# Performance work log

Measured on AMD Instinct MI355X. Metric: run time of the kernel, lower is better.

Reference implementation:

```python
import jax, jax.numpy as jnp
import numpy as np

KH, KW = 3, 3
PAD = 1
STRIDE = 1


def dht1(x):
    # 1D Discrete Hartley Transform along last axis: Re(FFT) - Im(FFT)
    f = jnp.fft.fft(x, axis=-1)
    return f.real - f.imag


def dht2(x, fft_h, fft_w):
    # zero-pad trailing two dims up to (fft_h, fft_w), then DHT along w then h
    pad_h = fft_h - x.shape[-2]
    pad_w = fft_w - x.shape[-1]
    pads = [(0, 0)] * (x.ndim - 2) + [(0, pad_h), (0, pad_w)]
    x = jnp.pad(x, pads)
    x = dht1(x)
    x = jnp.swapaxes(dht1(jnp.swapaxes(x, -1, -2)), -1, -2)
    return x


def setup_inputs() -> dict:
    key = jax.random.key(0)
    k1, k2 = jax.random.split(key)
    x = jax.random.normal(k1, (8, 64, 128, 128), dtype=jnp.float32)
    weight = jax.random.normal(k2, (64, 64, KH, KW), dtype=jnp.float32)
    return {"x": x, "weight": weight}


def reference(x, weight):
    b, c_in, h, w = x.shape
    out_h = (h + 2 * PAD - KH) // STRIDE + 1
    out_w = (w + 2 * PAD - KW) // STRIDE + 1
    x_p = jnp.pad(x, ((0, 0), (0, 0), (PAD, PAD), (PAD, PAD)))
    fft_h = h + 2 * PAD + KH - 1
    fft_w = w + 2 * PAD + KW - 1

    x_ht = dht2(x_p, fft_h, fft_w)          # [B, Cin, fh, fw]
    w_ht = dht2(weight, fft_h, fft_w)        # [Cout, Cin, fh, fw]

    x_f = jnp.flip(x_ht, axis=(-2, -1))
    w_f = jnp.flip(w_ht, axis=(-2, -1))

    # Fused combine + sum over Cin: avoids [B,Cout,Cin,fh,fw] intermediates.
    t1 = jnp.einsum('bchw,ochw->bohw', x_ht, w_ht)
    t2 = jnp.einsum('bchw,ochw->bohw', x_ht, w_f)
    t3 = jnp.einsum('bchw,ochw->bohw', x_f, w_ht)
    t4 = jnp.einsum('bchw,ochw->bohw', x_f, w_f)
    out_ht = (t1 + t2 + t3 - t4) * 0.5

    # idht2 in the source applies only the 1/n scaling twice (no transform)
    output = out_ht / jnp.asarray(fft_h * fft_w, dtype=out_ht.dtype)
    return output[:, :, :out_h, :out_w]
```

## Files before the change

### kernel.cpp

```cpp
#include <hip/hip_runtime.h>
#include <hip/hip_fp16.h>


#define SCALE (0.5f / 17424.0f)
#define MFMA  __builtin_amdgcn_mfma_f32_16x16x32_f16

typedef __attribute__((ext_vector_type(8))) _Float16 f16x8;
typedef __attribute__((ext_vector_type(4))) _Float16 f16x4;
typedef __attribute__((ext_vector_type(4))) float    f32x4;

__global__ __launch_bounds__(512, 4) void dht2_prep(
    const float* __restrict__ x, const float* __restrict__ w,
    _Float16* __restrict__ X, _Float16* __restrict__ cfT,
    _Float16* __restrict__ hgT)
{
    const int tid = threadIdx.x;
    const float step = 6.28318530717958647692f / 132.0f;

    if (blockIdx.x >= 512) {
        const int bid2 = blockIdx.x - 512;
        if (bid2 == 66) {
            if (tid < 128) {
                const int v = tid;
                float s, c;
                _Float16 o[8];
                o[0] = (_Float16)1.0f; o[3] = (_Float16)1.0f;
                o[6] = (_Float16)0.0f; o[7] = (_Float16)0.0f;
                sincosf((float)((v * 1) % 132) * step, &s, &c);       o[1] = (_Float16)(c + s);
                sincosf((float)((v * 2) % 132) * step, &s, &c);       o[2] = (_Float16)(c + s);
                sincosf((float)(((v + 1) * 1) % 132) * step, &s, &c); o[4] = (_Float16)(c - s);
                sincosf((float)(((v + 1) * 2) % 132) * step, &s, &c); o[5] = (_Float16)(c - s);
                *(f16x8*)(cfT + v * 8) = *(f16x8*)o;
            }
            return;
        }
        const int u = bid2;
        float a[3], ap[3];
        a[0] = 1.f; ap[0] = 1.f;
        #pragma unroll
        for (int i = 1; i < 3; ++i) {
            float s, c;
            sincosf((float)((u * i) % 132) * step, &s, &c);
            a[i] = c + s;
            sincosf((float)(((u + 1) * i) % 132) * step, &s, &c);
            ap[i] = c - s;
        }
        for (int it = 0; it < 8; ++it) {
            const int oc = it * 512 + tid;
            const float* wp = w + (size_t)oc * 9;
            float w9[9];
            #pragma unroll
            for (int q = 0; q < 9; ++q) w9[q] = wp[q];
            #pragma unroll
            for (int j = 0; j < 3; ++j) {
                const float h = a[0]*w9[j] + a[1]*w9[3+j] + a[2]*w9[6+j];
                const float g = ap[0]*w9[j] + ap[1]*w9[3+j] + ap[2]*w9[6+j];
                hgT[((size_t)u * 6 + j)     * 4096 + oc] = (_Float16)h;
                hgT[((size_t)u * 6 + 3 + j) * 4096 + oc] = (_Float16)g;
            }
        }
        return;
    }

    const int bc = blockIdx.x;
    const int wv = tid >> 6, lane = tid & 63;
    const int col = lane & 15, quad = lane >> 4;
    __shared__ _Float16 Tfl[144][136];
    __shared__ _Float16 Y1l[144][136];
    __shared__ float castab[132];

    const float* xp = x + (size_t)bc * 16384;
    const int ic = wv * 16 + col;

    float4 xv[4][2];
    #pragma unroll
    for (int kc = 0; kc < 4; ++kc) {
        const int k0 = kc * 32 + quad * 8;
        xv[kc][0] = *(const float4*)(xp + ic * 128 + k0);
        xv[kc][1] = *(const float4*)(xp + ic * 128 + k0 + 4);
    }
    if (tid < 132) {
        float s, c;
        sincosf((float)tid * step, &s, &c);
        castab[tid] = c + s;
    }
    __syncthreads();
    #pragma unroll
    for (int s = 0; s < 36; ++s) {
        const int idx = s * 512 + tid;
        const int row = idx >> 7;
        const int ci  = idx & 127;
        float v = 0.f;
        if (row < 132) v = castab[(row * (ci + 1)) % 132];
        Tfl[row][ci] = (_Float16)v;
    }
    f16x8 bfA[4];
    #pragma unroll
    for (int kc = 0; kc < 4; ++kc) {
        f16x8 t;
        t[0] = (_Float16)xv[kc][0].x; t[1] = (_Float16)xv[kc][0].y;
        t[2] = (_Float16)xv[kc][0].z; t[3] = (_Float16)xv[kc][0].w;
        t[4] = (_Float16)xv[kc][1].x; t[5] = (_Float16)xv[kc][1].y;
        t[6] = (_Float16)xv[kc][1].z; t[7] = (_Float16)xv[kc][1].w;
        bfA[kc] = t;
    }
    __syncthreads();

    f32x4 accA[9];
    #pragma unroll
    for (int mt = 0; mt < 9; ++mt) accA[mt] = (f32x4)0.f;
    #pragma unroll
    for (int kc = 0; kc < 4; ++kc) {
        const int k0 = kc * 32 + quad * 8;
        #pragma unroll
        for (int mt = 0; mt < 9; ++mt) {
            const f16x8 af = *(const f16x8*)&Tfl[mt * 16 + col][k0];
            accA[mt] = MFMA(af, bfA[kc], accA[mt], 0, 0, 0);
        }
    }
    #pragma unroll
    for (int mt = 0; mt < 9; ++mt)
        #pragma unroll
        for (int r = 0; r < 4; ++r)
            Y1l[mt * 16 + quad * 4 + r][ic] = (_Float16)accA[mt][r];
    __syncthreads();

    f32x4 accB[9];
    #pragma unroll
    for (int mt = 0; mt < 9; ++mt) accB[mt] = (f32x4)0.f;
    #pragma unroll
    for (int kc = 0; kc < 4; ++kc) {
        const int k0 = kc * 32 + quad * 8;
        const f16x8 bf = *(const f16x8*)&Y1l[wv * 16 + col][k0];
        #pragma unroll
        for (int mt = 0; mt < 9; ++mt) {
            const f16x8 af = *(const f16x8*)&Tfl[mt * 16 + col][k0];
            accB[mt] = MFMA(af, bf, accB[mt], 0, 0, 0);
        }
    }
    f32x4 accT[3];
    #pragma unroll
    for (int j = 0; j < 3; ++j) accT[j] = (f32x4)0.f;
    if (wv < 4) {
        #pragma unroll
        for (int kc = 0; kc < 4; ++kc) {
            const int k0 = kc * 32 + quad * 8;
            const f16x8 bf = *(const f16x8*)&Y1l[128 + col][k0];
            #pragma unroll
            for (int j = 0; j < 3; ++j) {
                if (j < 2 || wv == 0) {
                    const int mt = (j == 2) ? 8 : (wv * 2 + j);
                    const f16x8 af = *(const f16x8*)&Tfl[mt * 16 + col][k0];
                    accT[j] = MFMA(af, bf, accT[j], 0, 0, 0);
                }
            }
        }
    }
    __syncthreads();

    #pragma unroll
    for (int mt = 0; mt < 9; ++mt)
        #pragma unroll
        for (int r = 0; r < 4; ++r)
            Tfl[mt * 16 + quad * 4 + r][wv * 16 + col] = (_Float16)accB[mt][r];
    if (wv < 4 && col < 4) {
        #pragma unroll
        for (int j = 0; j < 3; ++j) {
            if (j < 2 || wv == 0) {
                const int mt = (j == 2) ? 8 : (wv * 2 + j);
                #pragma unroll
                for (int r = 0; r < 4; ++r)
                    Tfl[mt * 16 + quad * 4 + r][128 + col] = (_Float16)accT[j][r];
            }
        }
    }
    __syncthreads();
    _Float16* Xp = X + (size_t)bc * 17952;
    #pragma unroll
    for (int s = 0; s < 5; ++s) {
        const int ch = tid + 512 * s;
        if (ch < 2244) {
            const int u = ch / 17, kk = ch - u * 17;
            *(f16x8*)(Xp + u * 136 + kk * 8) = *(const f16x8*)&Tfl[u][kk * 8];
        }
    }
}

__global__ __launch_bounds__(256, 2) void combine_mfma(
    const _Float16* __restrict__ X, const _Float16* __restrict__ hgT,
    const _Float16* __restrict__ cfT, float* __restrict__ out)
{
    const int uidx = blockIdx.x;
    const int b = blockIdx.y;
    const int tid = threadIdx.x;
    const int wv = tid >> 6, lane = tid & 63;
    const int col = lane & 15, quad = lane >> 4;
    const int u2 = 131 - uidx;
    const bool doB = (uidx >= 4);

    __shared__ _Float16 Ps[132][72];
    __shared__ _Float16 Ms[132][72];

    {
        const int c = tid >> 2, sub = tid & 3;
        const _Float16* rowd = X + (size_t)(b * 64 + c) * 17952 + (size_t)uidx * 136;
        const _Float16* rowm = X + (size_t)(b * 64 + c) * 17952 + (size_t)u2 * 136;
        #pragma unroll
        for (int k = 0; k < 8; ++k) {
            const int v0 = sub * 32 + 4 * k;
            const f16x4 d = *(const f16x4*)(rowd + v0);
            const f16x4 m = *(const f16x4*)(rowm + (128 - v0));
            #pragma unroll
            for (int i = 0; i < 4; ++i) {
                Ps[v0 + i][c] = d[i] + m[3 - i];
                Ms[v0 + i][c] = d[i] - m[3 - i];
            }
        }
        if (sub == 0) {
            const f16x4 d = *(const f16x4*)(rowd + 128);
            const f16x4 m = *(const f16x4*)(rowm);
            #pragma unroll
            for (int i = 0; i < 4; ++i) {
                Ps[128 + i][c] = d[i] + m[3 - i];
                Ms[128 + i][c] = d[i] - m[3 - i];
            }
        }
    }

    const _Float16* hgu = hgT + (size_t)uidx * 6 * 4096;
    const int orow = wv * 16 + col;
    f16x8 hA[3][2], gA[3][2];
    #pragma unroll
    for (int kt = 0; kt < 3; ++kt)
        #pragma unroll
        for (int hf = 0; hf < 2; ++hf) {
            hA[kt][hf] = *(const f16x8*)(hgu + ((size_t)kt * 64 + orow) * 64 + hf * 32 + quad * 8);
            gA[kt][hf] = *(const f16x8*)(hgu + ((size_t)(3 + kt) * 64 + orow) * 64 + hf * 32 + quad * 8);
        }
    __syncthreads();

    float* outA = out + (((size_t)(b * 64 + wv * 16 + quad * 4)) * 128 + uidx) * 128 + col;
    float* outB = out + (((size_t)(b * 64 + wv * 16 + quad * 4)) * 128 + u2) * 128 + col;

    #pragma unroll
    for (int nt = 0; nt < 8; ++nt) {
        const int vA = nt * 16 + col;
        const int vB = 131 - vA;
        const f16x8 cf8 = *(const f16x8*)(cfT + (size_t)(nt * 16 + col) * 8);
        const float c1 = (float)cf8[1], c2 = (float)cf8[2];
        const float d1 = (float)cf8[4], d2 = (float)cf8[5];
        {
            const f16x8 p0 = *(const f16x8*)&Ps[vA][quad * 8];
            const f16x8 p1 = *(const f16x8*)&Ps[vA][32 + quad * 8];
            const f16x8 m0 = *(const f16x8*)&Ms[vA][quad * 8];
            const f16x8 m1 = *(const f16x8*)&Ms[vA][32 + quad * 8];
            f32x4 aP0 = (f32x4)0.f, aP1 = (f32x4)0.f, aP2 = (f32x4)0.f;
            f32x4 aM0 = (f32x4)0.f, aM1 = (f32x4)0.f, aM2 = (f32x4)0.f;
            aP0 = MFMA(hA[0][0], p0, aP0, 0, 0, 0); aP0 = MFMA(hA[0][1], p1, aP0, 0, 0, 0);
            aP1 = MFMA(hA[1][0], p0, aP1, 0, 0, 0); aP1 = MFMA(hA[1][1], p1, aP1, 0, 0, 0);
            aP2 = MFMA(hA[2][0], p0, aP2, 0, 0, 0); aP2 = MFMA(hA[2][1], p1, aP2, 0, 0, 0);
            aM0 = MFMA(gA[0][0], m0, aM0, 0, 0, 0); aM0 = MFMA(gA[0][1], m1, aM0, 0, 0, 0);
            aM1 = MFMA(gA[1][0], m0, aM1, 0, 0, 0); aM1 = MFMA(gA[1][1], m1, aM1, 0, 0, 0);
            aM2 = MFMA(gA[2][0], m0, aM2, 0, 0, 0); aM2 = MFMA(gA[2][1], m1, aM2, 0, 0, 0);
            #pragma unroll
            for (int r = 0; r < 4; ++r)
                outA[(size_t)r * 16384 + nt * 16] =
                    ((aP0[r] + c1 * aP1[r] + c2 * aP2[r]) +
                     (aM0[r] + d1 * aM1[r] + d2 * aM2[r])) * SCALE;
        }
        if (doB) {
            const f16x8 p0 = *(const f16x8*)&Ps[vB][quad * 8];
            const f16x8 p1 = *(const f16x8*)&Ps[vB][32 + quad * 8];
            const f16x8 m0 = *(const f16x8*)&Ms[vB][quad * 8];
            const f16x8 m1 = *(const f16x8*)&Ms[vB][32 + quad * 8];
            f32x4 bP0 = (f32x4)0.f, bP1 = (f32x4)0.f, bP2 = (f32x4)0.f;
            f32x4 bM0 = (f32x4)0.f, bM1 = (f32x4)0.f, bM2 = (f32x4)0.f;
            bP0 = MFMA(gA[0][0], p0, bP0, 0, 0, 0); bP0 = MFMA(gA[0][1], p1, bP0, 0, 0, 0);
            bP1 = MFMA(gA[1][0], p0, bP1, 0, 0, 0); bP1 = MFMA(gA[1][1], p1, bP1, 0, 0, 0);
            bP2 = MFMA(gA[2][0], p0, bP2, 0, 0, 0); bP2 = MFMA(gA[2][1], p1, bP2, 0, 0, 0);
            bM0 = MFMA(hA[0][0], m0, bM0, 0, 0, 0); bM0 = MFMA(hA[0][1], m1, bM0, 0, 0, 0);
            bM1 = MFMA(hA[1][0], m0, bM1, 0, 0, 0); bM1 = MFMA(hA[1][1], m1, bM1, 0, 0, 0);
            bM2 = MFMA(hA[2][0], m0, bM2, 0, 0, 0); bM2 = MFMA(hA[2][1], m1, bM2, 0, 0, 0);
            #pragma unroll
            for (int r = 0; r < 4; ++r)
                outB[(size_t)r * 16384 + nt * 16] =
                    ((bP0[r] + c1 * bP1[r] + c2 * bP2[r]) -
                     (bM0[r] + d1 * bM1[r] + d2 * bM2[r])) * SCALE;
        }
    }
}

extern "C" void kernel_launch(void* const* d_in, const int* in_sizes, int n_in,
                              void* d_out, int out_size, void* d_ws, size_t ws_size,
                              hipStream_t stream)
{
    const float* x = (const float*)d_in[0];
    const float* w = (const float*)d_in[1];
    char* ws = (char*)d_ws;
    _Float16* cfT = (_Float16*)(ws + 36864);
    _Float16* X   = (_Float16*)(ws + 65536);
    _Float16* hgT = (_Float16*)(ws + 18448384);

    dht2_prep<<<dim3(579), dim3(512), 0, stream>>>(x, w, X, cfT, hgT);

    combine_mfma<<<dim3(66, 8), dim3(256), 0, stream>>>(
        X, hgT, cfT, (float*)d_out);
}
```

Baseline: 110.7 us.

## Spread weight transform across image blocks and strength-reduce DHT table fill

Folds the separate weight-transform and twiddle-table blocks into the 512 image-transform blocks, so each block does one or two slices of the weight work instead of a few tail blocks doing eight slices each. Replaces the per-element modulo in the Hartley table fill with incremental index stepping. In the combine kernel it raises the launch-bounds occupancy hint and splits the mirrored-row pass into its own loop. The trade-off is extra work and register pressure in every prep block, and the higher occupancy hint may force register spills in the combine kernel.

New measurement: 114.1 us. 1.03x slower.

```diff
diff --git a/kernel.cpp b/kernel.cpp
--- a/kernel.cpp
+++ b/kernel.cpp
@@ -9,62 +9,44 @@
 typedef __attribute__((ext_vector_type(4))) _Float16 f16x4;
 typedef __attribute__((ext_vector_type(4))) float    f32x4;
 
-__global__ __launch_bounds__(512, 4) void dht2_prep(
+static __device__ __forceinline__ void prep_hg_unit(
+    int unit, int tid, const float* __restrict__ w, _Float16* __restrict__ hgT)
+{
+    const int u = unit >> 3, it = unit & 7;
+    const float step = 6.28318530717958647692f / 132.0f;
+    float a[3], ap[3];
+    a[0] = 1.f; ap[0] = 1.f;
+    #pragma unroll
+    for (int i = 1; i < 3; ++i) {
+        float s, c;
+        sincosf((float)((u * i) % 132) * step, &s, &c);
+        a[i] = c + s;
+        sincosf((float)(((u + 1) * i) % 132) * step, &s, &c);
+        ap[i] = c - s;
+    }
+    const int oc = it * 512 + tid;
+    const float* wp = w + (size_t)oc * 9;
+    float w9[9];
+    #pragma unroll
+    for (int q = 0; q < 9; ++q) w9[q] = wp[q];
+    #pragma unroll
+    for (int j = 0; j < 3; ++j) {
+        const float h = a[0]*w9[j] + a[1]*w9[3+j] + a[2]*w9[6+j];
+        const float g = ap[0]*w9[j] + ap[1]*w9[3+j] + ap[2]*w9[6+j];
+        hgT[((size_t)u * 6 + j)     * 4096 + oc] = (_Float16)h;
+        hgT[((size_t)u * 6 + 3 + j) * 4096 + oc] = (_Float16)g;
+    }
+}
+
+__global__ __launch_bounds__(512, 4) void dht2_all(
     const float* __restrict__ x, const float* __restrict__ w,
     _Float16* __restrict__ X, _Float16* __restrict__ cfT,
     _Float16* __restrict__ hgT)
 {
-    const int tid = threadIdx.x;
+    const int bc = blockIdx.x;
+    const int tid = threadIdx.x, wv = tid >> 6, lane = tid & 63;
+    const int col = lane & 15, quad = lane >> 4;
     const float step = 6.28318530717958647692f / 132.0f;
-
-    if (blockIdx.x >= 512) {
-        const int bid2 = blockIdx.x - 512;
-        if (bid2 == 66) {
-            if (tid < 128) {
-                const int v = tid;
-                float s, c;
-                _Float16 o[8];
-                o[0] = (_Float16)1.0f; o[3] = (_Float16)1.0f;
-                o[6] = (_Float16)0.0f; o[7] = (_Float16)0.0f;
-                sincosf((float)((v * 1) % 132) * step, &s, &c);       o[1] = (_Float16)(c + s);
-                sincosf((float)((v * 2) % 132) * step, &s, &c);       o[2] = (_Float16)(c + s);
-                sincosf((float)(((v + 1) * 1) % 132) * step, &s, &c); o[4] = (_Float16)(c - s);
-                sincosf((float)(((v + 1) * 2) % 132) * step, &s, &c); o[5] = (_Float16)(c - s);
-                *(f16x8*)(cfT + v * 8) = *(f16x8*)o;
-            }
-            return;
-        }
-        const int u = bid2;
-        float a[3], ap[3];
-        a[0] = 1.f; ap[0] = 1.f;
-        #pragma unroll
-        for (int i = 1; i < 3; ++i) {
-            float s, c;
-            sincosf((float)((u * i) % 132) * step, &s, &c);
-            a[i] = c + s;
-            sincosf((float)(((u + 1) * i) % 132) * step, &s, &c);
-            ap[i] = c - s;
-        }
-        for (int it = 0; it < 8; ++it) {
-            const int oc = it * 512 + tid;
-            const float* wp = w + (size_t)oc * 9;
-            float w9[9];
-            #pragma unroll
-            for (int q = 0; q < 9; ++q) w9[q] = wp[q];
-            #pragma unroll
-            for (int j = 0; j < 3; ++j) {
-                const float h = a[0]*w9[j] + a[1]*w9[3+j] + a[2]*w9[6+j];
-                const float g = ap[0]*w9[j] + ap[1]*w9[3+j] + ap[2]*w9[6+j];
-                hgT[((size_t)u * 6 + j)     * 4096 + oc] = (_Float16)h;
-                hgT[((size_t)u * 6 + 3 + j) * 4096 + oc] = (_Float16)g;
-            }
-        }
-        return;
-    }
-
-    const int bc = blockIdx.x;
-    const int wv = tid >> 6, lane = tid & 63;
-    const int col = lane & 15, quad = lane >> 4;
     __shared__ _Float16 Tfl[144][136];
     __shared__ _Float16 Y1l[144][136];
     __shared__ float castab[132];
@@ -79,20 +61,42 @@
         xv[kc][0] = *(const float4*)(xp + ic * 128 + k0);
         xv[kc][1] = *(const float4*)(xp + ic * 128 + k0 + 4);
     }
+
+    prep_hg_unit(bc, tid, w, hgT);
+    if (bc < 16) prep_hg_unit(512 + bc, tid, w, hgT);
+    if (bc == 16 && tid < 128) {
+        const int v = tid;
+        float s, c;
+        _Float16 o[8];
+        o[0] = (_Float16)1.0f; o[3] = (_Float16)1.0f;
+        o[6] = (_Float16)0.0f; o[7] = (_Float16)0.0f;
+        sincosf((float)((v * 1) % 132) * step, &s, &c);       o[1] = (_Float16)(c + s);
+        sincosf((float)((v * 2) % 132) * step, &s, &c);       o[2] = (_Float16)(c + s);
+        sincosf((float)(((v + 1) * 1) % 132) * step, &s, &c); o[4] = (_Float16)(c - s);
+        sincosf((float)(((v + 1) * 2) % 132) * step, &s, &c); o[5] = (_Float16)(c - s);
+        *(f16x8*)(cfT + v * 8) = *(f16x8*)o;
+    }
+
     if (tid < 132) {
         float s, c;
         sincosf((float)tid * step, &s, &c);
         castab[tid] = c + s;
     }
     __syncthreads();
-    #pragma unroll
-    for (int s = 0; s < 36; ++s) {
-        const int idx = s * 512 + tid;
-        const int row = idx >> 7;
-        const int ci  = idx & 127;
-        float v = 0.f;
-        if (row < 132) v = castab[(row * (ci + 1)) % 132];
-        Tfl[row][ci] = (_Float16)v;
+
+    {
+        const int ci = tid & 127;
+        const int row0 = tid >> 7;
+        int m  = (row0 * (ci + 1)) % 132;
+        int dm = (4 * (ci + 1)) % 132;
+        int row = row0;
+        #pragma unroll
+        for (int s = 0; s < 36; ++s) {
+            const float v = (row < 132) ? castab[m] : 0.f;
+            Tfl[row][ci] = (_Float16)v;
+            row += 4;
+            m += dm; if (m >= 132) m -= 132;
+        }
     }
     f16x8 bfA[4];
     #pragma unroll
@@ -186,7 +190,7 @@
     }
 }
 
-__global__ __launch_bounds__(256, 2) void combine_mfma(
+__global__ __launch_bounds__(256, 4) void combine_mfma(
     const _Float16* __restrict__ X, const _Float16* __restrict__ hgT,
     const _Float16* __restrict__ cfT, float* __restrict__ out)
 {
@@ -245,30 +249,35 @@
     #pragma unroll
     for (int nt = 0; nt < 8; ++nt) {
         const int vA = nt * 16 + col;
-        const int vB = 131 - vA;
         const f16x8 cf8 = *(const f16x8*)(cfT + (size_t)(nt * 16 + col) * 8);
         const float c1 = (float)cf8[1], c2 = (float)cf8[2];
         const float d1 = (float)cf8[4], d2 = (float)cf8[5];
-        {
-            const f16x8 p0 = *(const f16x8*)&Ps[vA][quad * 8];
-            const f16x8 p1 = *(const f16x8*)&Ps[vA][32 + quad * 8];
-            const f16x8 m0 = *(const f16x8*)&Ms[vA][quad * 8];
-            const f16x8 m1 = *(const f16x8*)&Ms[vA][32 + quad * 8];
-            f32x4 aP0 = (f32x4)0.f, aP1 = (f32x4)0.f, aP2 = (f32x4)0.f;
-            f32x4 aM0 = (f32x4)0.f, aM1 = (f32x4)0.f, aM2 = (f32x4)0.f;
-            aP0 = MFMA(hA[0][0], p0, aP0, 0, 0, 0); aP0 = MFMA(hA[0][1], p1, aP0, 0, 0, 0);
-            aP1 = MFMA(hA[1][0], p0, aP1, 0, 0, 0); aP1 = MFMA(hA[1][1], p1, aP1, 0, 0, 0);
-            aP2 = MFMA(hA[2][0], p0, aP2, 0, 0, 0); aP2 = MFMA(hA[2][1], p1, aP2, 0, 0, 0);
-            aM0 = MFMA(gA[0][0], m0, aM0, 0, 0, 0); aM0 = MFMA(gA[0][1], m1, aM0, 0, 0, 0);
-            aM1 = MFMA(gA[1][0], m0, aM1, 0, 0, 0); aM1 = MFMA(gA[1][1], m1, aM1, 0, 0, 0);
-            aM2 = MFMA(gA[2][0], m0, aM2, 0, 0, 0); aM2 = MFMA(gA[2][1], m1, aM2, 0, 0, 0);
-            #pragma unroll
-            for (int r = 0; r < 4; ++r)
-                outA[(size_t)r * 16384 + nt * 16] =
-                    ((aP0[r] + c1 * aP1[r] + c2 * aP2[r]) +
-                     (aM0[r] + d1 * aM1[r] + d2 * aM2[r])) * SCALE;
-        }
-        if (doB) {
+        const f16x8 p0 = *(const f16x8*)&Ps[vA][quad * 8];
+        const f16x8 p1 = *(const f16x8*)&Ps[vA][32 + quad * 8];
+        const f16x8 m0 = *(const f16x8*)&Ms[vA][quad * 8];
+        const f16x8 m1 = *(const f16x8*)&Ms[vA][32 + quad * 8];
+        f32x4 aP0 = (f32x4)0.f, aP1 = (f32x4)0.f, aP2 = (f32x4)0.f;
+        f32x4 aM0 = (f32x4)0.f, aM1 = (f32x4)0.f, aM2 = (f32x4)0.f;
+        aP0 = MFMA(hA[0][0], p0, aP0, 0, 0, 0); aP0 = MFMA(hA[0][1], p1, aP0, 0, 0, 0);
+        aP1 = MFMA(hA[1][0], p0, aP1, 0, 0, 0); aP1 = MFMA(hA[1][1], p1, aP1, 0, 0, 0);
+        aP2 = MFMA(hA[2][0], p0, aP2, 0, 0, 0); aP2 = MFMA(hA[2][1], p1, aP2, 0, 0, 0);
+        aM0 = MFMA(gA[0][0], m0, aM0, 0, 0, 0); aM0 = MFMA(gA[0][1], m1, aM0, 0, 0, 0);
+        aM1 = MFMA(gA[1][0], m0, aM1, 0, 0, 0); aM1 = MFMA(gA[1][1], m1, aM1, 0, 0, 0);
+        aM2 = MFMA(gA[2][0], m0, aM2, 0, 0, 0); aM2 = MFMA(gA[2][1], m1, aM2, 0, 0, 0);
+        #pragma unroll
+        for (int r = 0; r < 4; ++r)
+            outA[(size_t)r * 16384 + nt * 16] =
+                ((aP0[r] + c1 * aP1[r] + c2 * aP2[r]) +
+                 (aM0[r] + d1 * aM1[r] + d2 * aM2[r])) * SCALE;
+    }
+    if (doB) {
+        #pragma unroll
+        for (int nt = 0; nt < 8; ++nt) {
+            const int vA = nt * 16 + col;
+            const int vB = 131 - vA;
+            const f16x8 cf8 = *(const f16x8*)(cfT + (size_t)(nt * 16 + col) * 8);
+            const float c1 = (float)cf8[1], c2 = (float)cf8[2];
+            const float d1 = (float)cf8[4], d2 = (float)cf8[5];
             const f16x8 p0 = *(const f16x8*)&Ps[vB][quad * 8];
             const f16x8 p1 = *(const f16x8*)&Ps[vB][32 + quad * 8];
             const f16x8 m0 = *(const f16x8*)&Ms[vB][quad * 8];
@@ -301,7 +310,7 @@
     _Float16* X   = (_Float16*)(ws + 65536);
     _Float16* hgT = (_Float16*)(ws + 18448384);
 
-    dht2_prep<<<dim3(579), dim3(512), 0, stream>>>(x, w, X, cfT, hgT);
+    dht2_all<<<dim3(512), dim3(512), 0, stream>>>(x, w, X, cfT, hgT);
 
     combine_mfma<<<dim3(66, 8), dim3(256), 0, stream>>>(
         X, hgT, cfT, (float*)d_out);
```
